# Kernel tuning notes

Measured on AMD Instinct MI355X. Metric: run time of the kernel, lower is better.

## Reference

```python
import jax, jax.numpy as jnp
import numpy as np


def setup_inputs() -> dict:
    key = jax.random.key(0)
    k1, k2, k3, k4, k5 = jax.random.split(key, 5)
    b, l, h, dh, g, n = 2, 2048, 8, 64, 1, 64
    x = jax.random.normal(k1, (b, l, h, dh), dtype=jnp.float32)
    dt = jax.random.uniform(k2, (b, l, h), dtype=jnp.float32)
    # A must be negative (Mamba convention) so exp(segsum(A*dt)) is bounded
    A = -jnp.abs(jax.random.normal(k3, (h,), dtype=jnp.float32))
    B = jax.random.normal(k4, (b, l, g, n), dtype=jnp.float32)
    C = jax.random.normal(k5, (b, l, g, n), dtype=jnp.float32)
    return {"x": x, "dt": dt, "A": A, "B": B, "C": C, "chunk_size": 64}


def _forward(x, dt, A, B, C):
    b, l, h, dh = x.shape
    g = B.shape[2]
    rep = h // g
    # expand_groups_to_heads: repeat each group across its heads
    q = jnp.repeat(C, rep, axis=2).astype(jnp.float32)  # (b,l,h,n)
    k = jnp.repeat(B, rep, axis=2).astype(jnp.float32)  # (b,l,h,n)
    v = x.astype(jnp.float32)                            # (b,l,h,dh)
    adt = A * dt                                         # (b,l,h)

    # rotary on last dim; angles = cumsum(dt) broadcast over n//2 (NeoX half-split)
    half = q.shape[-1] // 2
    ang = jnp.cumsum(dt, axis=1)[..., None]              # (b,l,h,1)
    cos, sin = jnp.cos(ang), jnp.sin(ang)

    def rope(t):
        t1, t2 = t[..., :half], t[..., half:]
        return jnp.concatenate([t1 * cos - t2 * sin, t1 * sin + t2 * cos], axis=-1)

    q, k = rope(q), rope(k)

    # segsum decay: decay[b,h,l,s] = exp(sum_{s<t<=l} adt_t) for s<=l else 0
    a = adt.transpose(0, 2, 1)                           # (b,h,l)
    cs = jnp.cumsum(a, axis=-1)
    seg = cs[..., :, None] - cs[..., None, :]            # (b,h,l,l)
    causal = jnp.tril(jnp.ones((l, l), dtype=bool))
    decay = jnp.where(causal, jnp.exp(seg), 0.0)

    # trapezoidal scale with trap=0 (baseline passes zeros): w_s = 0.5*(1+exp(adt_s))
    w = 0.5 * (1.0 + jnp.exp(a))                         # (b,h,l)
    decay = decay * w[..., None, :]                      # scale each key position s

    scores = jnp.einsum('blhd,bshd->bhls', q, k) * decay
    y = jnp.einsum('bhls,bshd->blhd', scores, v)
    return y


def reference(x, dt, A, B, C, chunk_size):
    # chunk_size is unused by the quadratic (non-chunked) reference formulation
    return _forward(x, dt, A, B, C)
```

## Files before the change

kernel.cpp:

```cpp
#include <hip/hip_runtime.h>
#include <math.h>

constexpr int L_ = 2048;
constexpr int H_ = 8;
constexpr int BH_ = 16;
constexpr int TSZ = 64;
constexpr int NT_ = L_ / TSZ;
constexpr int CHUNK = 8;
constexpr int NCHP = NT_ / CHUNK;
constexpr float SKIP_THR = -15.f;

typedef __bf16 bf16x8 __attribute__((ext_vector_type(8)));
typedef __bf16 bf16x4 __attribute__((ext_vector_type(4)));
typedef float f32x4 __attribute__((ext_vector_type(4)));

constexpr size_t ANG_OFF = 0;
constexpr size_t SN_OFF  = ANG_OFF + (size_t)BH_ * L_;
constexpr size_t CS_OFF  = SN_OFF  + (size_t)BH_ * L_;
constexpr size_t SNW_OFF = CS_OFF  + (size_t)BH_ * L_;
constexpr size_t CSW_OFF = SNW_OFF + (size_t)BH_ * L_;
constexpr size_t PART_OFF = CSW_OFF + (size_t)BH_ * L_;

__device__ __forceinline__ int swz(int row, int d) {
    return row * 64 + ((((d >> 3) ^ (row & 7))) << 3) + (d & 7);
}

__global__ void scan_kernel(const float* __restrict__ dt, const float* __restrict__ A,
                            float* __restrict__ ws) {
    int bh = blockIdx.x;
    int b = bh >> 3, h = bh & 7;
    int t = threadIdx.x;
    __shared__ float part[256];
    const float* dtp = dt + (size_t)b * L_ * H_ + h;
    float v[8];
    float s = 0.f;
    int l0 = t * 8;
#pragma unroll
    for (int i = 0; i < 8; ++i) { v[i] = dtp[(size_t)(l0 + i) * H_]; s += v[i]; }
    part[t] = s;
    __syncthreads();
#pragma unroll
    for (int off = 1; off < 256; off <<= 1) {
        float add = (t >= off) ? part[t - off] : 0.f;
        __syncthreads();
        part[t] += add;
        __syncthreads();
    }
    float run = (t == 0) ? 0.f : part[t - 1];
    float Ah = A[h];
    size_t base = (size_t)bh * L_ + l0;
#pragma unroll
    for (int i = 0; i < 8; ++i) {
        run += v[i];
        float sn, cs;
        sincosf(run, &sn, &cs);
        float w = 0.5f * (1.f + __expf(Ah * v[i]));
        ws[ANG_OFF + base + i] = run;
        ws[SN_OFF  + base + i] = sn;
        ws[CS_OFF  + base + i] = cs;
        ws[SNW_OFF + base + i] = sn * w;
        ws[CSW_OFF + base + i] = cs * w;
    }
}

__launch_bounds__(256)
__global__ void attn_kernel(const float* __restrict__ x, const float* __restrict__ A,
                            const float* __restrict__ Bm, const float* __restrict__ Cm,
                            float* __restrict__ ws, float* __restrict__ out) {
    int rt = blockIdx.x, bh = blockIdx.y, cz = blockIdx.z;
    bool diag = (cz == 0);
    int b = bh >> 3, h = bh & 7;
    float Ah = A[h];
    int l0 = rt * TSZ;
    const float* angB = ws + ANG_OFF + (size_t)bh * L_;
    const float* snA  = ws + SN_OFF  + (size_t)bh * L_;
    const float* csA  = ws + CS_OFF  + (size_t)bh * L_;
    const float* snwA = ws + SNW_OFF + (size_t)bh * L_;
    const float* cswA = ws + CSW_OFF + (size_t)bh * L_;
    float angL0 = angB[l0];

    auto pred = [&](int st) {
        return Ah * (angL0 - angB[(size_t)st * TSZ + TSZ - 1]) >= SKIP_THR;
    };
    int st_first = rt - 1 - cz * CHUNK;
    int st_lo = st_first - (CHUNK - 1);
    if (!diag && (st_first < 0 || !pred(st_first))) return;
    bool solo = diag && ((rt - 1 - CHUNK < 0) || !pred(rt - 1 - CHUNK));

    __shared__ __align__(16) __bf16 lds_q[64 * 64];
    __shared__ __align__(16) __bf16 lds_k[64 * 64];
    __shared__ __align__(16) __bf16 lds_vt[64 * 72];
    __shared__ __align__(16) __bf16 lds_p[64 * 64];
    __shared__ float angRow[TSZ];
    __shared__ float colfac[TSZ];

    int t = threadIdx.x;
    int w = t >> 6, lane = t & 63, lg = lane >> 4, l15 = lane & 15;

    const float4* B4 = (const float4*)(Bm + (size_t)b * L_ * 64);
    const float4* C4 = (const float4*)(Cm + (size_t)b * L_ * 64);

#pragma unroll
    for (int it = 0; it < 2; ++it) {
        int wi = it * 256 + t;
        int r = wi >> 3, dq = wi & 7;
        int l = l0 + r;
        float4 lo = C4[(size_t)l * 16 + dq];
        float4 hi = C4[(size_t)l * 16 + dq + 8];
        float sn = snA[l], cs = csA[l];
        bf16x4 qlo = {(__bf16)(lo.x * cs - hi.x * sn), (__bf16)(lo.y * cs - hi.y * sn),
                      (__bf16)(lo.z * cs - hi.z * sn), (__bf16)(lo.w * cs - hi.w * sn)};
        bf16x4 qhi = {(__bf16)(lo.x * sn + hi.x * cs), (__bf16)(lo.y * sn + hi.y * cs),
                      (__bf16)(lo.z * sn + hi.z * cs), (__bf16)(lo.w * sn + hi.w * cs)};
        *(bf16x4*)&lds_q[swz(r, dq * 4)] = qlo;
        *(bf16x4*)&lds_q[swz(r, dq * 4 + 32)] = qhi;
    }
    if (t < TSZ) angRow[t] = angB[l0 + t];

    float4 pBlo[2], pBhi[2], pV[4];
    float pSnw[2], pCsw[2], pAng = 0.f;
    int sq = t >> 4, dqx = t & 15;

    auto prefetch = [&](int s0) {
#pragma unroll
        for (int it = 0; it < 2; ++it) {
            int wi = it * 256 + t;
            int r = wi >> 3, dq = wi & 7;
            int l = s0 + r;
            pBlo[it] = B4[(size_t)l * 16 + dq];
            pBhi[it] = B4[(size_t)l * 16 + dq + 8];
            pSnw[it] = snwA[l];
            pCsw[it] = cswA[l];
        }
        const float4* xv4 = (const float4*)(x + (((size_t)b * L_ + s0) * H_ + h) * 64);
#pragma unroll
        for (int i = 0; i < 4; ++i)
            pV[i] = xv4[(size_t)(sq * 4 + i) * 128 + dqx];
        if (t < TSZ) pAng = angB[s0 + t];
    };

    auto commit = [&]() {
#pragma unroll
        for (int it = 0; it < 2; ++it) {
            int wi = it * 256 + t;
            int r = wi >> 3, dq = wi & 7;
            float sw = pSnw[it], cw = pCsw[it];
            float4 lo = pBlo[it], hi = pBhi[it];
            bf16x4 klo = {(__bf16)(lo.x * cw - hi.x * sw), (__bf16)(lo.y * cw - hi.y * sw),
                          (__bf16)(lo.z * cw - hi.z * sw), (__bf16)(lo.w * cw - hi.w * sw)};
            bf16x4 khi = {(__bf16)(lo.x * sw + hi.x * cw), (__bf16)(lo.y * sw + hi.y * cw),
                          (__bf16)(lo.z * sw + hi.z * cw), (__bf16)(lo.w * sw + hi.w * cw)};
            *(bf16x4*)&lds_k[swz(r, dq * 4)] = klo;
            *(bf16x4*)&lds_k[swz(r, dq * 4 + 32)] = khi;
        }
#pragma unroll
        for (int j = 0; j < 4; ++j) {
            int d = dqx * 4 + j;
            bf16x4 vv = {(__bf16)((const float*)&pV[0])[j], (__bf16)((const float*)&pV[1])[j],
                         (__bf16)((const float*)&pV[2])[j], (__bf16)((const float*)&pV[3])[j]};
            *(bf16x4*)&lds_vt[d * 72 + sq * 4] = vv;
        }
        if (t < TSZ) colfac[t] = __expf(fminf(Ah * (angL0 - pAng), 0.f));
    };

    f32x4 accD[4] = {{0.f, 0.f, 0.f, 0.f}, {0.f, 0.f, 0.f, 0.f},
                     {0.f, 0.f, 0.f, 0.f}, {0.f, 0.f, 0.f, 0.f}};
    f32x4 accO[4] = {{0.f, 0.f, 0.f, 0.f}, {0.f, 0.f, 0.f, 0.f},
                     {0.f, 0.f, 0.f, 0.f}, {0.f, 0.f, 0.f, 0.f}};

    int qrow = w * 16 + l15;
    int rbase = w * 16 + lg * 4;

    auto s_mfma = [&](f32x4 (&sa)[4]) {
        bf16x8 a0 = *(const bf16x8*)&lds_q[swz(qrow, lg * 8)];
        bf16x8 a1 = *(const bf16x8*)&lds_q[swz(qrow, lg * 8 + 32)];
#pragma unroll
        for (int ng = 0; ng < 4; ++ng) {
            int srow = ng * 16 + l15;
            bf16x8 b0 = *(const bf16x8*)&lds_k[swz(srow, lg * 8)];
            bf16x8 b1 = *(const bf16x8*)&lds_k[swz(srow, lg * 8 + 32)];
            f32x4 z = {0.f, 0.f, 0.f, 0.f};
            z = __builtin_amdgcn_mfma_f32_16x16x32_bf16(a0, b0, z, 0, 0, 0);
            z = __builtin_amdgcn_mfma_f32_16x16x32_bf16(a1, b1, z, 0, 0, 0);
            sa[ng] = z;
        }
    };

    auto p_write = [&](f32x4 (&sa)[4]) {
#pragma unroll
        for (int ng = 0; ng < 4; ++ng)
#pragma unroll
            for (int reg = 0; reg < 4; ++reg)
                lds_p[swz(rbase + reg, ng * 16 + l15)] = (__bf16)sa[ng][reg];
    };

    auto pv_mfma = [&](f32x4 (&acc)[4]) {
        bf16x8 pa0 = *(const bf16x8*)&lds_p[swz(qrow, lg * 8)];
        bf16x8 pa1 = *(const bf16x8*)&lds_p[swz(qrow, lg * 8 + 32)];
#pragma unroll
        for (int ng = 0; ng < 4; ++ng) {
            int dl = ng * 16 + l15;
            bf16x8 v0 = *(const bf16x8*)&lds_vt[dl * 72 + lg * 8];
            bf16x8 v1 = *(const bf16x8*)&lds_vt[dl * 72 + lg * 8 + 32];
            acc[ng] = __builtin_amdgcn_mfma_f32_16x16x32_bf16(pa0, v0, acc[ng], 0, 0, 0);
            acc[ng] = __builtin_amdgcn_mfma_f32_16x16x32_bf16(pa1, v1, acc[ng], 0, 0, 0);
        }
    };

    int st;
    bool have_next;
    if (diag) {
        prefetch(l0);
        commit();
        st = rt - 1;
        have_next = (st >= 0) && pred(st);
        if (have_next) prefetch(st * TSZ);
        __syncthreads();
        f32x4 sa[4];
        s_mfma(sa);
        float ar[4];
#pragma unroll
        for (int reg = 0; reg < 4; ++reg) ar[reg] = angRow[rbase + reg];
#pragma unroll
        for (int ng = 0; ng < 4; ++ng) {
            int sl = ng * 16 + l15;
            float as = angRow[sl];
#pragma unroll
            for (int reg = 0; reg < 4; ++reg) {
                float dec = (sl <= rbase + reg) ? __expf(Ah * (ar[reg] - as)) : 0.f;
                sa[ng][reg] *= dec;
            }
        }
        p_write(sa);
        pv_mfma(accD);
    } else {
        st = st_first;
        have_next = true;
        prefetch(st * TSZ);
    }

    int st_end = (st_lo > 0) ? st_lo : 0;
    while (have_next) {
        __syncthreads();
        commit();
        int nst = st - 1;
        bool hn = (nst >= st_end) && pred(nst);
        if (hn) prefetch(nst * TSZ);
        __syncthreads();
        f32x4 sa[4];
        s_mfma(sa);
#pragma unroll
        for (int ng = 0; ng < 4; ++ng) {
            float cf = colfac[ng * 16 + l15];
#pragma unroll
            for (int reg = 0; reg < 4; ++reg) sa[ng][reg] *= cf;
        }
        p_write(sa);
        pv_mfma(accO);
        st = nst;
        have_next = hn;
    }

    if (solo) {
        float* op = out + (((size_t)b * L_ + l0) * H_ + h) * 64;
#pragma unroll
        for (int reg = 0; reg < 4; ++reg) {
            int rloc = rbase + reg;
            float rf = __expf(Ah * (angRow[rloc] - angL0));
#pragma unroll
            for (int ng = 0; ng < 4; ++ng)
                op[(size_t)rloc * H_ * 64 + ng * 16 + l15] =
                    accD[ng][reg] + rf * accO[ng][reg];
        }
    } else {
        float* pp = ws + PART_OFF + ((((size_t)rt * BH_ + bh) * NCHP + cz) << 12);
#pragma unroll
        for (int reg = 0; reg < 4; ++reg) {
            int rloc = rbase + reg;
            float rf = __expf(Ah * (angRow[rloc] - angL0));
#pragma unroll
            for (int ng = 0; ng < 4; ++ng)
                pp[(size_t)rloc * 64 + ng * 16 + l15] = accD[ng][reg] + rf * accO[ng][reg];
        }
    }
}

__launch_bounds__(256)
__global__ void reduce_kernel(const float* __restrict__ ws, const float* __restrict__ A,
                              float* __restrict__ out) {
    int rt = blockIdx.x, bh = blockIdx.y;
    int b = bh >> 3, h = bh & 7;
    float Ah = A[h];
    const float* angB = ws + ANG_OFF + (size_t)bh * L_;
    int l0 = rt * TSZ;
    float angL0 = angB[l0];
    auto pred = [&](int st) {
        return Ah * (angL0 - angB[(size_t)st * TSZ + TSZ - 1]) >= SKIP_THR;
    };
    if ((rt - 1 - CHUNK < 0) || !pred(rt - 1 - CHUNK)) return;

    int t = threadIdx.x;
    int r0 = (t >> 4) * 4, c0 = (t & 15) * 4;
    float acc[4][4] = {{0.f}};
    for (int cz = 0; cz < NCHP; ++cz) {
        if (cz > 0) {
            int st_first = rt - 1 - cz * CHUNK;
            if (st_first < 0 || !pred(st_first)) break;
        }
        const float* pp = ws + PART_OFF + ((((size_t)rt * BH_ + bh) * NCHP + cz) << 12);
#pragma unroll
        for (int i = 0; i < 4; ++i) {
            float4 v = *(const float4*)&pp[(size_t)(r0 + i) * 64 + c0];
            acc[i][0] += v.x; acc[i][1] += v.y; acc[i][2] += v.z; acc[i][3] += v.w;
        }
    }
    float* op = out + (((size_t)b * L_ + l0) * H_ + h) * 64;
#pragma unroll
    for (int i = 0; i < 4; ++i)
        *(float4*)&op[(size_t)(r0 + i) * H_ * 64 + c0] =
            make_float4(acc[i][0], acc[i][1], acc[i][2], acc[i][3]);
}

extern "C" void kernel_launch(void* const* d_in, const int* in_sizes, int n_in,
                              void* d_out, int out_size, void* d_ws, size_t ws_size,
                              hipStream_t stream) {
    const float* x  = (const float*)d_in[0];
    const float* dt = (const float*)d_in[1];
    const float* A  = (const float*)d_in[2];
    const float* Bm = (const float*)d_in[3];
    const float* Cm = (const float*)d_in[4];
    float* ws = (float*)d_ws;
    float* out = (float*)d_out;

    scan_kernel<<<BH_, 256, 0, stream>>>(dt, A, ws);
    attn_kernel<<<dim3(NT_, BH_, NCHP), 256, 0, stream>>>(x, A, Bm, Cm, ws, out);
    reduce_kernel<<<dim3(NT_, BH_), 256, 0, stream>>>(ws, A, out);
}
```

Baseline: 102.0 us.

## Double-buffer K/V tiles in LDS to drop one barrier per iteration

K, transposed V and the column decay factors move into two-slot LDS buffers. Each iteration now writes the next tile into the spare slot while computing on the current one, so each loop step needs one block-wide barrier instead of two. The diagonal tile and the off-diagonal tiles are merged into one unified loop. This costs more LDS per block, which may reduce occupancy.

```diff
diff --git a/kernel.cpp b/kernel.cpp
--- a/kernel.cpp
+++ b/kernel.cpp
@@ -83,16 +83,17 @@
         return Ah * (angL0 - angB[(size_t)st * TSZ + TSZ - 1]) >= SKIP_THR;
     };
     int st_first = rt - 1 - cz * CHUNK;
-    int st_lo = st_first - (CHUNK - 1);
     if (!diag && (st_first < 0 || !pred(st_first))) return;
+    int st_end = st_first - (CHUNK - 1);
+    if (st_end < 0) st_end = 0;
     bool solo = diag && ((rt - 1 - CHUNK < 0) || !pred(rt - 1 - CHUNK));
 
     __shared__ __align__(16) __bf16 lds_q[64 * 64];
-    __shared__ __align__(16) __bf16 lds_k[64 * 64];
-    __shared__ __align__(16) __bf16 lds_vt[64 * 72];
+    __shared__ __align__(16) __bf16 lds_k[2][64 * 64];
+    __shared__ __align__(16) __bf16 lds_vt[2][64 * 72];
     __shared__ __align__(16) __bf16 lds_p[64 * 64];
     __shared__ float angRow[TSZ];
-    __shared__ float colfac[TSZ];
+    __shared__ float colfac[2][TSZ];
 
     int t = threadIdx.x;
     int w = t >> 6, lane = t & 63, lg = lane >> 4, l15 = lane & 15;
@@ -139,7 +140,7 @@
         if (t < TSZ) pAng = angB[s0 + t];
     };
 
-    auto commit = [&]() {
+    auto commit = [&](int p) {
 #pragma unroll
         for (int it = 0; it < 2; ++it) {
             int wi = it * 256 + t;
@@ -150,17 +151,17 @@
                           (__bf16)(lo.z * cw - hi.z * sw), (__bf16)(lo.w * cw - hi.w * sw)};
             bf16x4 khi = {(__bf16)(lo.x * sw + hi.x * cw), (__bf16)(lo.y * sw + hi.y * cw),
                           (__bf16)(lo.z * sw + hi.z * cw), (__bf16)(lo.w * sw + hi.w * cw)};
-            *(bf16x4*)&lds_k[swz(r, dq * 4)] = klo;
-            *(bf16x4*)&lds_k[swz(r, dq * 4 + 32)] = khi;
+            *(bf16x4*)&lds_k[p][swz(r, dq * 4)] = klo;
+            *(bf16x4*)&lds_k[p][swz(r, dq * 4 + 32)] = khi;
         }
 #pragma unroll
         for (int j = 0; j < 4; ++j) {
             int d = dqx * 4 + j;
             bf16x4 vv = {(__bf16)((const float*)&pV[0])[j], (__bf16)((const float*)&pV[1])[j],
                          (__bf16)((const float*)&pV[2])[j], (__bf16)((const float*)&pV[3])[j]};
-            *(bf16x4*)&lds_vt[d * 72 + sq * 4] = vv;
-        }
-        if (t < TSZ) colfac[t] = __expf(fminf(Ah * (angL0 - pAng), 0.f));
+            *(bf16x4*)&lds_vt[p][d * 72 + sq * 4] = vv;
+        }
+        if (t < TSZ) colfac[p][t] = __expf(fminf(Ah * (angL0 - pAng), 0.f));
     };
 
     f32x4 accD[4] = {{0.f, 0.f, 0.f, 0.f}, {0.f, 0.f, 0.f, 0.f},
@@ -171,14 +172,14 @@
     int qrow = w * 16 + l15;
     int rbase = w * 16 + lg * 4;
 
-    auto s_mfma = [&](f32x4 (&sa)[4]) {
+    auto s_mfma = [&](int p, f32x4 (&sa)[4]) {
         bf16x8 a0 = *(const bf16x8*)&lds_q[swz(qrow, lg * 8)];
         bf16x8 a1 = *(const bf16x8*)&lds_q[swz(qrow, lg * 8 + 32)];
 #pragma unroll
         for (int ng = 0; ng < 4; ++ng) {
             int srow = ng * 16 + l15;
-            bf16x8 b0 = *(const bf16x8*)&lds_k[swz(srow, lg * 8)];
-            bf16x8 b1 = *(const bf16x8*)&lds_k[swz(srow, lg * 8 + 32)];
+            bf16x8 b0 = *(const bf16x8*)&lds_k[p][swz(srow, lg * 8)];
+            bf16x8 b1 = *(const bf16x8*)&lds_k[p][swz(srow, lg * 8 + 32)];
             f32x4 z = {0.f, 0.f, 0.f, 0.f};
             z = __builtin_amdgcn_mfma_f32_16x16x32_bf16(a0, b0, z, 0, 0, 0);
             z = __builtin_amdgcn_mfma_f32_16x16x32_bf16(a1, b1, z, 0, 0, 0);
@@ -194,71 +195,77 @@
                 lds_p[swz(rbase + reg, ng * 16 + l15)] = (__bf16)sa[ng][reg];
     };
 
-    auto pv_mfma = [&](f32x4 (&acc)[4]) {
+    auto pv_mfma = [&](int p, f32x4 (&acc)[4]) {
         bf16x8 pa0 = *(const bf16x8*)&lds_p[swz(qrow, lg * 8)];
         bf16x8 pa1 = *(const bf16x8*)&lds_p[swz(qrow, lg * 8 + 32)];
 #pragma unroll
         for (int ng = 0; ng < 4; ++ng) {
             int dl = ng * 16 + l15;
-            bf16x8 v0 = *(const bf16x8*)&lds_vt[dl * 72 + lg * 8];
-            bf16x8 v1 = *(const bf16x8*)&lds_vt[dl * 72 + lg * 8 + 32];
+            bf16x8 v0 = *(const bf16x8*)&lds_vt[p][dl * 72 + lg * 8];
+            bf16x8 v1 = *(const bf16x8*)&lds_vt[p][dl * 72 + lg * 8 + 32];
             acc[ng] = __builtin_amdgcn_mfma_f32_16x16x32_bf16(pa0, v0, acc[ng], 0, 0, 0);
             acc[ng] = __builtin_amdgcn_mfma_f32_16x16x32_bf16(pa1, v1, acc[ng], 0, 0, 0);
         }
     };
 
-    int st;
-    bool have_next;
-    if (diag) {
-        prefetch(l0);
-        commit();
-        st = rt - 1;
-        have_next = (st >= 0) && pred(st);
-        if (have_next) prefetch(st * TSZ);
+    int gen_st = diag ? (rt - 1) : (st_first - 1);
+    auto next_s0 = [&]() -> int {
+        if (gen_st < st_end || !pred(gen_st)) return -1;
+        int s = gen_st * TSZ;
+        --gen_st;
+        return s;
+    };
+
+    int cur = diag ? l0 : st_first * TSZ;
+    prefetch(cur);
+    commit(0);
+    int nxt = next_s0();
+    if (nxt >= 0) prefetch(nxt);
+    __syncthreads();
+
+    int p = 0;
+    bool first = true;
+    while (true) {
+        int nn = -1;
+        if (nxt >= 0) {
+            commit(p ^ 1);
+            nn = next_s0();
+            if (nn >= 0) prefetch(nn);
+        }
+        f32x4 sa[4];
+        s_mfma(p, sa);
+        if (first && diag) {
+            float ar[4];
+#pragma unroll
+            for (int reg = 0; reg < 4; ++reg) ar[reg] = angRow[rbase + reg];
+#pragma unroll
+            for (int ng = 0; ng < 4; ++ng) {
+                int sl = ng * 16 + l15;
+                float as = angRow[sl];
+#pragma unroll
+                for (int reg = 0; reg < 4; ++reg) {
+                    float dec = (sl <= rbase + reg) ? __expf(Ah * (ar[reg] - as)) : 0.f;
+                    sa[ng][reg] *= dec;
+                }
+            }
+            p_write(sa);
+            pv_mfma(p, accD);
+        } else {
+#pragma unroll
+            for (int ng = 0; ng < 4; ++ng) {
+                float cf = colfac[p][ng * 16 + l15];
+#pragma unroll
+                for (int reg = 0; reg < 4; ++reg) sa[ng][reg] *= cf;
+            }
+            p_write(sa);
+            pv_mfma(p, accO);
+        }
+        first = false;
+        if (nxt < 0) break;
         __syncthreads();
-        f32x4 sa[4];
-        s_mfma(sa);
-        float ar[4];
-#pragma unroll
-        for (int reg = 0; reg < 4; ++reg) ar[reg] = angRow[rbase + reg];
-#pragma unroll
-        for (int ng = 0; ng < 4; ++ng) {
-            int sl = ng * 16 + l15;
-            float as = angRow[sl];
-#pragma unroll
-            for (int reg = 0; reg < 4; ++reg) {
-                float dec = (sl <= rbase + reg) ? __expf(Ah * (ar[reg] - as)) : 0.f;
-                sa[ng][reg] *= dec;
-            }
-        }
-        p_write(sa);
-        pv_mfma(accD);
-    } else {
-        st = st_first;
-        have_next = true;
-        prefetch(st * TSZ);
-    }
-
-    int st_end = (st_lo > 0) ? st_lo : 0;
-    while (have_next) {
-        __syncthreads();
-        commit();
-        int nst = st - 1;
-        bool hn = (nst >= st_end) && pred(nst);
-        if (hn) prefetch(nst * TSZ);
-        __syncthreads();
-        f32x4 sa[4];
-        s_mfma(sa);
-#pragma unroll
-        for (int ng = 0; ng < 4; ++ng) {
-            float cf = colfac[ng * 16 + l15];
-#pragma unroll
-            for (int reg = 0; reg < 4; ++reg) sa[ng][reg] *= cf;
-        }
-        p_write(sa);
-        pv_mfma(accO);
-        st = nst;
-        have_next = hn;
+        p ^= 1;
+        cur = nxt;
+        nxt = nn;
     }
 
     if (solo) {
```

Measured after the change: 101.5 us. About the same (-0.5%).
